# Kernel optimization log

Hardware: AMD Instinct MI355X
Metric: run time of the kernel (lower is better)

## Reference

```python
import jax, jax.numpy as jnp
import numpy as np

B, C, H, W = 8, 512, 96, 96
CQ = 64  # inter_ch


def setup_inputs() -> dict:
    key = jax.random.key(0)
    ks = jax.random.split(key, 8)
    scale = 1.0 / np.sqrt(C)
    return {
        "x": jax.random.normal(ks[0], (B, C, H, W), dtype=jnp.float32),
        "Wq": jax.random.normal(ks[1], (CQ, C), dtype=jnp.float32) * scale,
        "bq": jax.random.normal(ks[2], (CQ,), dtype=jnp.float32) * 0.01,
        "Wk": jax.random.normal(ks[3], (CQ, C), dtype=jnp.float32) * scale,
        "bk": jax.random.normal(ks[4], (CQ,), dtype=jnp.float32) * 0.01,
        "Wv": jax.random.normal(ks[5], (C, C), dtype=jnp.float32) * scale,
        "bv": jax.random.normal(ks[6], (C,), dtype=jnp.float32) * 0.01,
        "gamma": jax.random.normal(ks[7], (1,), dtype=jnp.float32) * 0.1,
    }


def reference(x, Wq, bq, Wk, bk, Wv, bv, gamma):
    # 1x1 convs expressed as channel matmuls; outputs in BHWC layout
    Q = jnp.einsum('bchw,oc->bhwo', x, Wq) + bq   # [B,H,W,CQ]
    K = jnp.einsum('bchw,oc->bhwo', x, Wk) + bk   # [B,H,W,CQ]
    V = jnp.einsum('bchw,oc->bhwo', x, Wv) + bv   # [B,H,W,C]

    # Per pixel (i,j): keys = concat(row i keys [W], column j keys [H]).
    # NOTE: this replication includes pixel (i,j) twice (once in row, once in col),
    # matching the torch loop exactly (no -INF masking as in original CCNet).
    e_row = jnp.einsum('bhwc,bhvc->bhwv', Q, K)   # [B,H,W,W] attend along row h
    e_col = jnp.einsum('bhwc,bgwc->bhwg', Q, K)   # [B,H,W,H] attend along col w
    attn = jax.nn.softmax(jnp.concatenate([e_row, e_col], axis=-1), axis=-1)
    a_row, a_col = attn[..., :W], attn[..., W:]   # [B,H,W,W], [B,H,W,H]

    out = (jnp.einsum('bhwv,bhvc->bhwc', a_row, V)
           + jnp.einsum('bhwg,bgwc->bhwc', a_col, V))  # [B,H,W,C]
    out = jnp.transpose(out, (0, 3, 1, 2))        # [B,C,H,W]
    return x + gamma[0] * out
```

## Files before the change

kernel.cpp:

```cpp
#include <hip/hip_runtime.h>
#include <stdint.h>

#define B_  8
#define C_  512
#define H_  96
#define W_  96
#define CQ_ 64
#define P_  (H_*W_)
#define NP  (B_*P_)
#define L_  (W_+H_)

typedef __attribute__((ext_vector_type(8))) short short8;
typedef __attribute__((ext_vector_type(4))) float f32x4;

__device__ __forceinline__ ushort f2bf(float f) {
    uint32_t u = __builtin_bit_cast(uint32_t, f);
    u += 0x7fff + ((u >> 16) & 1);
    return (ushort)(u >> 16);
}
__device__ __forceinline__ float bf2f(ushort h) {
    uint32_t u = ((uint32_t)h) << 16;
    return __builtin_bit_cast(float, u);
}

__global__ __launch_bounds__(256) void k_xt(const float* __restrict__ x, ushort* __restrict__ xt) {
    __shared__ float tile[64][65];
    int p0 = blockIdx.x * 64, c0 = blockIdx.y * 64, bat = blockIdx.z;
    int tx = threadIdx.x, ty = threadIdx.y;
    const float* xb = x + ((size_t)bat * C_ + c0) * P_ + p0;
    #pragma unroll
    for (int i = ty; i < 64; i += 4) tile[i][tx] = xb[(size_t)i * P_ + tx];
    __syncthreads();
    ushort* o = xt + ((size_t)bat * P_ + p0) * C_ + c0;
    #pragma unroll
    for (int i = ty; i < 64; i += 4) o[(size_t)i * C_ + tx] = f2bf(tile[tx][i]);
}

__global__ __launch_bounds__(256) void k_wconv(const float* __restrict__ Wq, const float* __restrict__ Wk,
                                               const float* __restrict__ Wv, ushort* __restrict__ Wall) {
    int idx = blockIdx.x * 256 + threadIdx.x;
    if (idx >= 640 * C_) return;
    int o = idx / C_, c = idx % C_;
    float v;
    if (o < 64)       v = Wq[o * C_ + c];
    else if (o < 128) v = Wk[(o - 64) * C_ + c];
    else              v = Wv[(o - 128) * C_ + c];
    Wall[idx] = f2bf(v);
}

#define LSTR 40
__global__ __launch_bounds__(256) void k_qk(const ushort* __restrict__ xt, const ushort* __restrict__ Wall,
                                            const float* __restrict__ bq, const float* __restrict__ bk,
                                            ushort* __restrict__ Qb, ushort* __restrict__ Kb) {
    __shared__ __align__(16) ushort Al[128 * LSTR];
    __shared__ __align__(16) ushort Bl[128 * LSTR];
    int tid = threadIdx.x, lane = tid & 63, wvid = tid >> 6;
    int wr = wvid >> 1, wc = wvid & 1;
    int r0 = blockIdx.x * 128;
    f32x4 acc[4][4] = {};
    for (int kb = 0; kb < C_; kb += 32) {
        #pragma unroll
        for (int s = 0; s < 2; ++s) {
            int idx = tid + s * 256, row = idx >> 2, seg = idx & 3;
            *(short8*)&Al[row * LSTR + seg * 8] = *(const short8*)&xt[(size_t)(r0 + row) * C_ + kb + seg * 8];
            *(short8*)&Bl[row * LSTR + seg * 8] = *(const short8*)&Wall[(size_t)row * C_ + kb + seg * 8];
        }
        __syncthreads();
        int rr = lane & 15, gq = lane >> 4;
        #pragma unroll
        for (int mt = 0; mt < 4; ++mt) {
            short8 fa = *(const short8*)&Al[(wr * 64 + mt * 16 + rr) * LSTR + gq * 8];
            #pragma unroll
            for (int nt = 0; nt < 4; ++nt) {
                short8 fb = *(const short8*)&Bl[(wc * 64 + nt * 16 + rr) * LSTR + gq * 8];
                acc[mt][nt] = __builtin_amdgcn_mfma_f32_16x16x32_bf16(fa, fb, acc[mt][nt], 0, 0, 0);
            }
        }
        __syncthreads();
    }
    int rr = lane & 15, gq = lane >> 4;
    #pragma unroll
    for (int mt = 0; mt < 4; ++mt)
        #pragma unroll
        for (int nt = 0; nt < 4; ++nt) {
            int o = wc * 64 + nt * 16 + rr;
            #pragma unroll
            for (int q = 0; q < 4; ++q) {
                size_t prow = (size_t)r0 + wr * 64 + mt * 16 + gq * 4 + q;
                float v = acc[mt][nt][q];
                if (o < 64) Qb[prow * CQ_ + o]        = f2bf(v + bq[o]);
                else        Kb[prow * CQ_ + (o - 64)] = f2bf(v + bk[o - 64]);
            }
        }
}

__global__ __launch_bounds__(256) void k_v(const ushort* __restrict__ xt, const ushort* __restrict__ Wall,
                                           const float* __restrict__ bv, ushort* __restrict__ Vcm) {
    __shared__ __align__(16) ushort Al[128 * LSTR];
    __shared__ __align__(16) ushort Bl[128 * LSTR];
    int tid = threadIdx.x, lane = tid & 63, wvid = tid >> 6;
    int wr = wvid >> 1, wc = wvid & 1;
    int n0 = blockIdx.x * 128;
    int m0 = blockIdx.y * 128;
    f32x4 acc[4][4] = {};
    for (int kb = 0; kb < C_; kb += 32) {
        #pragma unroll
        for (int s = 0; s < 2; ++s) {
            int idx = tid + s * 256, row = idx >> 2, seg = idx & 3;
            *(short8*)&Al[row * LSTR + seg * 8] = *(const short8*)&Wall[(size_t)(128 + m0 + row) * C_ + kb + seg * 8];
            *(short8*)&Bl[row * LSTR + seg * 8] = *(const short8*)&xt[(size_t)(n0 + row) * C_ + kb + seg * 8];
        }
        __syncthreads();
        int rr = lane & 15, gq = lane >> 4;
        #pragma unroll
        for (int mt = 0; mt < 4; ++mt) {
            short8 fa = *(const short8*)&Al[(wr * 64 + mt * 16 + rr) * LSTR + gq * 8];
            #pragma unroll
            for (int nt = 0; nt < 4; ++nt) {
                short8 fb = *(const short8*)&Bl[(wc * 64 + nt * 16 + rr) * LSTR + gq * 8];
                acc[mt][nt] = __builtin_amdgcn_mfma_f32_16x16x32_bf16(fa, fb, acc[mt][nt], 0, 0, 0);
            }
        }
        __syncthreads();
    }
    int rr = lane & 15, gq = lane >> 4;
    int bat = n0 / P_, pb = n0 % P_;
    #pragma unroll
    for (int mt = 0; mt < 4; ++mt)
        #pragma unroll
        for (int nt = 0; nt < 4; ++nt) {
            int pl = pb + wc * 64 + nt * 16 + rr;
            #pragma unroll
            for (int q = 0; q < 4; ++q) {
                int c = m0 + wr * 64 + mt * 16 + gq * 4 + q;
                Vcm[((size_t)(bat * C_ + c)) * P_ + pl] = f2bf(acc[mt][nt][q] + bv[c]);
            }
        }
}

__global__ __launch_bounds__(256) void k_vt(const ushort* __restrict__ Vcm, ushort* __restrict__ Vt) {
    __shared__ ushort t[32][33];
    int tile = blockIdx.x; int h0 = (tile / 3) * 32, w0 = (tile % 3) * 32;
    int c = blockIdx.y, bat = blockIdx.z;
    int tx = threadIdx.x, ty = threadIdx.y;
    const ushort* src = Vcm + ((size_t)(bat * C_ + c)) * P_;
    #pragma unroll
    for (int i = ty; i < 32; i += 8) t[i][tx] = src[(h0 + i) * W_ + w0 + tx];
    __syncthreads();
    #pragma unroll
    for (int i = ty; i < 32; i += 8)
        Vt[((size_t)(bat * W_ + w0 + i) * C_ + c) * H_ + h0 + tx] = t[tx][i];
}

__global__ __launch_bounds__(256) void k_erow(const ushort* __restrict__ Qb, const ushort* __restrict__ Kb,
                                              float* __restrict__ logits) {
    __shared__ __align__(16) ushort Al[96 * LSTR];
    __shared__ __align__(16) ushort Bl[96 * LSTR];
    int h = blockIdx.x, bat = blockIdx.y;
    int tid = threadIdx.x, lane = tid & 63, wvid = tid >> 6;
    int wr = wvid >> 1, wc = wvid & 1;
    size_t base = ((size_t)bat * H_ + h) * W_;
    f32x4 acc[3][3] = {};
    for (int kb = 0; kb < CQ_; kb += 32) {
        for (int s = tid; s < 96 * 4; s += 256) {
            int row = s >> 2, seg = s & 3;
            *(short8*)&Al[row * LSTR + seg * 8] = *(const short8*)&Qb[(base + row) * CQ_ + kb + seg * 8];
            *(short8*)&Bl[row * LSTR + seg * 8] = *(const short8*)&Kb[(base + row) * CQ_ + kb + seg * 8];
        }
        __syncthreads();
        int rr = lane & 15, gq = lane >> 4;
        #pragma unroll
        for (int mt = 0; mt < 3; ++mt) {
            short8 fa = *(const short8*)&Al[(wr * 48 + mt * 16 + rr) * LSTR + gq * 8];
            #pragma unroll
            for (int nt = 0; nt < 3; ++nt) {
                short8 fb = *(const short8*)&Bl[(wc * 48 + nt * 16 + rr) * LSTR + gq * 8];
                acc[mt][nt] = __builtin_amdgcn_mfma_f32_16x16x32_bf16(fa, fb, acc[mt][nt], 0, 0, 0);
            }
        }
        __syncthreads();
    }
    int rr = lane & 15, gq = lane >> 4;
    #pragma unroll
    for (int mt = 0; mt < 3; ++mt)
        #pragma unroll
        for (int nt = 0; nt < 3; ++nt)
            #pragma unroll
            for (int q = 0; q < 4; ++q) {
                int w = wr * 48 + mt * 16 + gq * 4 + q;
                int v = wc * 48 + nt * 16 + rr;
                logits[(base + w) * L_ + v] = acc[mt][nt][q];
            }
}

__global__ __launch_bounds__(256) void k_ecol(const ushort* __restrict__ Qb, const ushort* __restrict__ Kb,
                                              float* __restrict__ logits) {
    __shared__ __align__(16) ushort Al[96 * LSTR];
    __shared__ __align__(16) ushort Bl[96 * LSTR];
    int w = blockIdx.x, bat = blockIdx.y;
    int tid = threadIdx.x, lane = tid & 63, wvid = tid >> 6;
    int wr = wvid >> 1, wc = wvid & 1;
    f32x4 acc[3][3] = {};
    for (int kb = 0; kb < CQ_; kb += 32) {
        for (int s = tid; s < 96 * 4; s += 256) {
            int row = s >> 2, seg = s & 3;
            size_t px = ((size_t)bat * H_ + row) * W_ + w;
            *(short8*)&Al[row * LSTR + seg * 8] = *(const short8*)&Qb[px * CQ_ + kb + seg * 8];
            *(short8*)&Bl[row * LSTR + seg * 8] = *(const short8*)&Kb[px * CQ_ + kb + seg * 8];
        }
        __syncthreads();
        int rr = lane & 15, gq = lane >> 4;
        #pragma unroll
        for (int mt = 0; mt < 3; ++mt) {
            short8 fa = *(const short8*)&Al[(wr * 48 + mt * 16 + rr) * LSTR + gq * 8];
            #pragma unroll
            for (int nt = 0; nt < 3; ++nt) {
                short8 fb = *(const short8*)&Bl[(wc * 48 + nt * 16 + rr) * LSTR + gq * 8];
                acc[mt][nt] = __builtin_amdgcn_mfma_f32_16x16x32_bf16(fa, fb, acc[mt][nt], 0, 0, 0);
            }
        }
        __syncthreads();
    }
    int rr = lane & 15, gq = lane >> 4;
    #pragma unroll
    for (int mt = 0; mt < 3; ++mt)
        #pragma unroll
        for (int nt = 0; nt < 3; ++nt)
            #pragma unroll
            for (int q = 0; q < 4; ++q) {
                int hh = wr * 48 + mt * 16 + gq * 4 + q;
                int gg = wc * 48 + nt * 16 + rr;
                logits[(((size_t)bat * H_ + hh) * W_ + w) * L_ + W_ + gg] = acc[mt][nt][q];
            }
}

__global__ __launch_bounds__(256) void k_softmax(const float* __restrict__ logits, ushort* __restrict__ attn) {
    int wvid = threadIdx.x >> 6, lane = threadIdx.x & 63;
    size_t px = (size_t)blockIdx.x * 4 + wvid;
    const float* lp = logits + px * L_;
    float v0 = lp[lane], v1 = lp[lane + 64], v2 = lp[lane + 128];
    float m = fmaxf(fmaxf(v0, v1), v2);
    #pragma unroll
    for (int off = 32; off; off >>= 1) m = fmaxf(m, __shfl_xor(m, off));
    float e0 = __expf(v0 - m), e1 = __expf(v1 - m), e2 = __expf(v2 - m);
    float s = e0 + e1 + e2;
    #pragma unroll
    for (int off = 32; off; off >>= 1) s += __shfl_xor(s, off);
    float inv = 1.0f / s;
    ushort* ap = attn + px * L_;
    ap[lane] = f2bf(e0 * inv); ap[lane + 64] = f2bf(e1 * inv); ap[lane + 128] = f2bf(e2 * inv);
}

__global__ __launch_bounds__(256) void k_pvrow(const ushort* __restrict__ Vcm, const ushort* __restrict__ attn,
                                               ushort* __restrict__ out0) {
    __shared__ __align__(16) ushort Al[128 * LSTR];
    __shared__ __align__(16) ushort Bl[96 * LSTR];
    int h = blockIdx.x, ct = blockIdx.y, bat = blockIdx.z;
    int tid = threadIdx.x, lane = tid & 63, wvid = tid >> 6;
    int wr = wvid >> 1, wc = wvid & 1;
    int c0 = ct * 128;
    size_t vbase = ((size_t)bat * C_ + c0) * P_ + (size_t)h * W_;
    size_t abase = (((size_t)bat * H_ + h) * W_) * L_;
    f32x4 acc[4][3] = {};
    for (int kb = 0; kb < 96; kb += 32) {
        for (int s = tid; s < 512; s += 256) {
            int row = s >> 2, seg = s & 3;
            *(short8*)&Al[row * LSTR + seg * 8] = *(const short8*)&Vcm[vbase + (size_t)row * P_ + kb + seg * 8];
        }
        for (int s = tid; s < 384; s += 256) {
            int row = s >> 2, seg = s & 3;
            *(short8*)&Bl[row * LSTR + seg * 8] = *(const short8*)&attn[abase + (size_t)row * L_ + kb + seg * 8];
        }
        __syncthreads();
        int rr = lane & 15, gq = lane >> 4;
        #pragma unroll
        for (int mt = 0; mt < 4; ++mt) {
            short8 fa = *(const short8*)&Al[(wr * 64 + mt * 16 + rr) * LSTR + gq * 8];
            #pragma unroll
            for (int nt = 0; nt < 3; ++nt) {
                short8 fb = *(const short8*)&Bl[(wc * 48 + nt * 16 + rr) * LSTR + gq * 8];
                acc[mt][nt] = __builtin_amdgcn_mfma_f32_16x16x32_bf16(fa, fb, acc[mt][nt], 0, 0, 0);
            }
        }
        __syncthreads();
    }
    int rr = lane & 15, gq = lane >> 4;
    #pragma unroll
    for (int mt = 0; mt < 4; ++mt)
        #pragma unroll
        for (int nt = 0; nt < 3; ++nt)
            #pragma unroll
            for (int q = 0; q < 4; ++q) {
                int c = c0 + wr * 64 + mt * 16 + gq * 4 + q;
                int w = wc * 48 + nt * 16 + rr;
                out0[((size_t)bat * C_ + c) * P_ + (size_t)h * W_ + w] = f2bf(acc[mt][nt][q]);
            }
}

__global__ __launch_bounds__(256) void k_pvcol(const ushort* __restrict__ Vt, const ushort* __restrict__ attn,
                                               ushort* __restrict__ out1) {
    __shared__ __align__(16) ushort Al[96 * LSTR];
    __shared__ __align__(16) ushort Bl[128 * LSTR];
    int w = blockIdx.x, ct = blockIdx.y, bat = blockIdx.z;
    int tid = threadIdx.x, lane = tid & 63, wvid = tid >> 6;
    int wr = wvid >> 1, wc = wvid & 1;
    int c0 = ct * 128;
    size_t abase = (((size_t)bat * H_) * W_ + w) * L_ + W_;
    size_t vbase = (((size_t)bat * W_ + w) * C_ + c0) * (size_t)H_;
    f32x4 acc[3][4] = {};
    for (int kb = 0; kb < 96; kb += 32) {
        for (int s = tid; s < 384; s += 256) {
            int row = s >> 2, seg = s & 3;
            *(short8*)&Al[row * LSTR + seg * 8] = *(const short8*)&attn[abase + (size_t)row * (W_ * L_) + kb + seg * 8];
        }
        for (int s = tid; s < 512; s += 256) {
            int row = s >> 2, seg = s & 3;
            *(short8*)&Bl[row * LSTR + seg * 8] = *(const short8*)&Vt[vbase + (size_t)row * H_ + kb + seg * 8];
        }
        __syncthreads();
        int rr = lane & 15, gq = lane >> 4;
        #pragma unroll
        for (int mt = 0; mt < 3; ++mt) {
            short8 fa = *(const short8*)&Al[(wr * 48 + mt * 16 + rr) * LSTR + gq * 8];
            #pragma unroll
            for (int nt = 0; nt < 4; ++nt) {
                short8 fb = *(const short8*)&Bl[(wc * 64 + nt * 16 + rr) * LSTR + gq * 8];
                acc[mt][nt] = __builtin_amdgcn_mfma_f32_16x16x32_bf16(fa, fb, acc[mt][nt], 0, 0, 0);
            }
        }
        __syncthreads();
    }
    int rr = lane & 15, gq = lane >> 4;
    #pragma unroll
    for (int mt = 0; mt < 3; ++mt)
        #pragma unroll
        for (int nt = 0; nt < 4; ++nt)
            #pragma unroll
            for (int q = 0; q < 4; ++q) {
                int hh = wr * 48 + mt * 16 + gq * 4 + q;
                int cc = c0 + wc * 64 + nt * 16 + rr;
                out1[(((size_t)bat * H_ + hh) * W_ + w) * C_ + cc] = f2bf(acc[mt][nt][q]);
            }
}

__global__ __launch_bounds__(256) void k_final(const float* __restrict__ x, const ushort* __restrict__ out0,
                                               const ushort* __restrict__ out1, const float* __restrict__ gamma,
                                               float* __restrict__ out) {
    __shared__ float t[32][33];
    int p0 = blockIdx.x * 32, c0 = blockIdx.y * 32, bat = blockIdx.z;
    int tx = threadIdx.x, ty = threadIdx.y;
    #pragma unroll
    for (int i = ty; i < 32; i += 8)
        t[i][tx] = bf2f(out1[((size_t)bat * P_ + p0 + i) * C_ + c0 + tx]);
    __syncthreads();
    float gm = gamma[0];
    #pragma unroll
    for (int i = ty; i < 32; i += 8) {
        size_t idx = ((size_t)bat * C_ + c0 + i) * P_ + p0 + tx;
        out[idx] = x[idx] + gm * (bf2f(out0[idx]) + t[tx][i]);
    }
}

extern "C" void kernel_launch(void* const* d_in, const int* in_sizes, int n_in,
                              void* d_out, int out_size, void* d_ws, size_t ws_size,
                              hipStream_t stream) {
    const float* x     = (const float*)d_in[0];
    const float* Wq    = (const float*)d_in[1];
    const float* bq    = (const float*)d_in[2];
    const float* Wk    = (const float*)d_in[3];
    const float* bk    = (const float*)d_in[4];
    const float* Wv    = (const float*)d_in[5];
    const float* bv    = (const float*)d_in[6];
    const float* gamma = (const float*)d_in[7];
    float* out = (float*)d_out;
    char* ws = (char*)d_ws;

    const size_t SZ = (size_t)NP * C_ * 2;
    ushort* Qb     = (ushort*)(ws);
    ushort* Kb     = (ushort*)(ws + (size_t)NP * CQ_ * 2);
    float*  logits = (float*) (ws + (size_t)NP * CQ_ * 4);
    ushort* out1   = (ushort*)(ws);
    ushort* xt     = (ushort*)(ws + SZ);
    ushort* out0   = xt;
    ushort* Vcm    = (ushort*)(ws + 2 * SZ);
    ushort* Vt     = (ushort*)(ws + 3 * SZ);
    ushort* attn   = (ushort*)(ws + 4 * SZ);
    ushort* Wall   = (ushort*)(ws + 4 * SZ + (size_t)NP * L_ * 2);

    k_xt     <<<dim3(144, 8, 8),  dim3(64, 4), 0, stream>>>(x, xt);
    k_wconv  <<<dim3(1280),       dim3(256),   0, stream>>>(Wq, Wk, Wv, Wall);
    k_qk     <<<dim3(576),        dim3(256),   0, stream>>>(xt, Wall, bq, bk, Qb, Kb);
    k_v      <<<dim3(576, 4),     dim3(256),   0, stream>>>(xt, Wall, bv, Vcm);
    k_vt     <<<dim3(9, 512, 8),  dim3(32, 8), 0, stream>>>(Vcm, Vt);
    k_erow   <<<dim3(96, 8),      dim3(256),   0, stream>>>(Qb, Kb, logits);
    k_ecol   <<<dim3(96, 8),      dim3(256),   0, stream>>>(Qb, Kb, logits);
    k_softmax<<<dim3(NP / 4),     dim3(256),   0, stream>>>(logits, attn);
    k_pvrow  <<<dim3(96, 4, 8),   dim3(256),   0, stream>>>(Vcm, attn, out0);
    k_pvcol  <<<dim3(96, 4, 8),   dim3(256),   0, stream>>>(Vt, attn, out1);
    k_final  <<<dim3(288, 16, 8), dim3(32, 8), 0, stream>>>(x, out0, out1, gamma, out);
}
```

Baseline: 429.2 us.

## Fuse Q/K/V projections into one GEMM and widen PV tiles to full channels

Merges the separate QK and V projection GEMMs into a single 512-thread kernel that computes all 640 output channels per pixel tile, so xt is read once, and adds a small transpose kernel to restore pixel-major Q/K. The PV row/col kernels now cover all 512 channels per block, which reuses the attention tile across channels. The column output is written channel-major so the final epilogue reads it with a per-channel LDS transpose and vectorized float2 accesses. The xt transpose is also vectorized. The trade-offs are a large accumulator array (10x4 per wave) that raises register pressure, and an extra launch plus the Q/K round trip through memory.

```diff
diff --git a/kernel.cpp b/kernel.cpp
--- a/kernel.cpp
+++ b/kernel.cpp
@@ -29,16 +29,31 @@
     int tx = threadIdx.x, ty = threadIdx.y;
     const float* xb = x + ((size_t)bat * C_ + c0) * P_ + p0;
     #pragma unroll
-    for (int i = ty; i < 64; i += 4) tile[i][tx] = xb[(size_t)i * P_ + tx];
+    for (int i = ty; i < 64; i += 8) {
+        float2 v = *(const float2*)&xb[(size_t)i * P_ + 2 * tx];
+        tile[i][2 * tx] = v.x; tile[i][2 * tx + 1] = v.y;
+    }
     __syncthreads();
     ushort* o = xt + ((size_t)bat * P_ + p0) * C_ + c0;
     #pragma unroll
-    for (int i = ty; i < 64; i += 4) o[(size_t)i * C_ + tx] = f2bf(tile[tx][i]);
+    for (int i = ty; i < 64; i += 8) {
+        ushort2 v; v.x = f2bf(tile[2 * tx][i]); v.y = f2bf(tile[2 * tx + 1][i]);
+        *(ushort2*)&o[(size_t)i * C_ + 2 * tx] = v;
+    }
 }
 
 __global__ __launch_bounds__(256) void k_wconv(const float* __restrict__ Wq, const float* __restrict__ Wk,
-                                               const float* __restrict__ Wv, ushort* __restrict__ Wall) {
+                                               const float* __restrict__ Wv, const float* __restrict__ bq,
+                                               const float* __restrict__ bk, const float* __restrict__ bv,
+                                               ushort* __restrict__ Wall, float* __restrict__ ball) {
     int idx = blockIdx.x * 256 + threadIdx.x;
+    if (idx < 640) {
+        float b;
+        if (idx < 64)       b = bq[idx];
+        else if (idx < 128) b = bk[idx - 64];
+        else                b = bv[idx - 128];
+        ball[idx] = b;
+    }
     if (idx >= 640 * C_) return;
     int o = idx / C_, c = idx % C_;
     float v;
@@ -49,93 +64,70 @@
 }
 
 #define LSTR 40
-__global__ __launch_bounds__(256) void k_qk(const ushort* __restrict__ xt, const ushort* __restrict__ Wall,
-                                            const float* __restrict__ bq, const float* __restrict__ bk,
-                                            ushort* __restrict__ Qb, ushort* __restrict__ Kb) {
-    __shared__ __align__(16) ushort Al[128 * LSTR];
+__global__ __launch_bounds__(512) void k_qkv(const ushort* __restrict__ xt, const ushort* __restrict__ Wall,
+                                             const float* __restrict__ ball,
+                                             ushort* __restrict__ Qcm, ushort* __restrict__ Kcm,
+                                             ushort* __restrict__ Vcm) {
+    __shared__ __align__(16) ushort Al[640 * LSTR];
     __shared__ __align__(16) ushort Bl[128 * LSTR];
     int tid = threadIdx.x, lane = tid & 63, wvid = tid >> 6;
-    int wr = wvid >> 1, wc = wvid & 1;
+    int wrm = wvid >> 1, wcn = wvid & 1;
     int r0 = blockIdx.x * 128;
-    f32x4 acc[4][4] = {};
+    f32x4 acc[10][4] = {};
     for (int kb = 0; kb < C_; kb += 32) {
         #pragma unroll
-        for (int s = 0; s < 2; ++s) {
-            int idx = tid + s * 256, row = idx >> 2, seg = idx & 3;
-            *(short8*)&Al[row * LSTR + seg * 8] = *(const short8*)&xt[(size_t)(r0 + row) * C_ + kb + seg * 8];
-            *(short8*)&Bl[row * LSTR + seg * 8] = *(const short8*)&Wall[(size_t)row * C_ + kb + seg * 8];
+        for (int s = 0; s < 5; ++s) {
+            int idx = tid + s * 512, row = idx >> 2, seg = idx & 3;
+            *(short8*)&Al[row * LSTR + seg * 8] = *(const short8*)&Wall[(size_t)row * C_ + kb + seg * 8];
+        }
+        {
+            int row = tid >> 2, seg = tid & 3;
+            *(short8*)&Bl[row * LSTR + seg * 8] = *(const short8*)&xt[(size_t)(r0 + row) * C_ + kb + seg * 8];
         }
         __syncthreads();
         int rr = lane & 15, gq = lane >> 4;
-        #pragma unroll
-        for (int mt = 0; mt < 4; ++mt) {
-            short8 fa = *(const short8*)&Al[(wr * 64 + mt * 16 + rr) * LSTR + gq * 8];
-            #pragma unroll
-            for (int nt = 0; nt < 4; ++nt) {
-                short8 fb = *(const short8*)&Bl[(wc * 64 + nt * 16 + rr) * LSTR + gq * 8];
-                acc[mt][nt] = __builtin_amdgcn_mfma_f32_16x16x32_bf16(fa, fb, acc[mt][nt], 0, 0, 0);
-            }
+        short8 fb[4];
+        #pragma unroll
+        for (int nt = 0; nt < 4; ++nt) fb[nt] = *(const short8*)&Bl[(wcn * 64 + nt * 16 + rr) * LSTR + gq * 8];
+        #pragma unroll
+        for (int mt = 0; mt < 10; ++mt) {
+            short8 fa = *(const short8*)&Al[(wrm * 160 + mt * 16 + rr) * LSTR + gq * 8];
+            #pragma unroll
+            for (int nt = 0; nt < 4; ++nt)
+                acc[mt][nt] = __builtin_amdgcn_mfma_f32_16x16x32_bf16(fa, fb[nt], acc[mt][nt], 0, 0, 0);
         }
         __syncthreads();
     }
     int rr = lane & 15, gq = lane >> 4;
-    #pragma unroll
-    for (int mt = 0; mt < 4; ++mt)
+    int bat = r0 / P_, pb = r0 % P_;
+    #pragma unroll
+    for (int mt = 0; mt < 10; ++mt)
         #pragma unroll
         for (int nt = 0; nt < 4; ++nt) {
-            int o = wc * 64 + nt * 16 + rr;
+            int col = wcn * 64 + nt * 16 + rr;
             #pragma unroll
             for (int q = 0; q < 4; ++q) {
-                size_t prow = (size_t)r0 + wr * 64 + mt * 16 + gq * 4 + q;
-                float v = acc[mt][nt][q];
-                if (o < 64) Qb[prow * CQ_ + o]        = f2bf(v + bq[o]);
-                else        Kb[prow * CQ_ + (o - 64)] = f2bf(v + bk[o - 64]);
-            }
-        }
-}
-
-__global__ __launch_bounds__(256) void k_v(const ushort* __restrict__ xt, const ushort* __restrict__ Wall,
-                                           const float* __restrict__ bv, ushort* __restrict__ Vcm) {
-    __shared__ __align__(16) ushort Al[128 * LSTR];
-    __shared__ __align__(16) ushort Bl[128 * LSTR];
-    int tid = threadIdx.x, lane = tid & 63, wvid = tid >> 6;
-    int wr = wvid >> 1, wc = wvid & 1;
-    int n0 = blockIdx.x * 128;
-    int m0 = blockIdx.y * 128;
-    f32x4 acc[4][4] = {};
-    for (int kb = 0; kb < C_; kb += 32) {
-        #pragma unroll
-        for (int s = 0; s < 2; ++s) {
-            int idx = tid + s * 256, row = idx >> 2, seg = idx & 3;
-            *(short8*)&Al[row * LSTR + seg * 8] = *(const short8*)&Wall[(size_t)(128 + m0 + row) * C_ + kb + seg * 8];
-            *(short8*)&Bl[row * LSTR + seg * 8] = *(const short8*)&xt[(size_t)(n0 + row) * C_ + kb + seg * 8];
-        }
-        __syncthreads();
-        int rr = lane & 15, gq = lane >> 4;
-        #pragma unroll
-        for (int mt = 0; mt < 4; ++mt) {
-            short8 fa = *(const short8*)&Al[(wr * 64 + mt * 16 + rr) * LSTR + gq * 8];
-            #pragma unroll
-            for (int nt = 0; nt < 4; ++nt) {
-                short8 fb = *(const short8*)&Bl[(wc * 64 + nt * 16 + rr) * LSTR + gq * 8];
-                acc[mt][nt] = __builtin_amdgcn_mfma_f32_16x16x32_bf16(fa, fb, acc[mt][nt], 0, 0, 0);
-            }
-        }
-        __syncthreads();
-    }
-    int rr = lane & 15, gq = lane >> 4;
-    int bat = n0 / P_, pb = n0 % P_;
-    #pragma unroll
-    for (int mt = 0; mt < 4; ++mt)
-        #pragma unroll
-        for (int nt = 0; nt < 4; ++nt) {
-            int pl = pb + wc * 64 + nt * 16 + rr;
-            #pragma unroll
-            for (int q = 0; q < 4; ++q) {
-                int c = m0 + wr * 64 + mt * 16 + gq * 4 + q;
-                Vcm[((size_t)(bat * C_ + c)) * P_ + pl] = f2bf(acc[mt][nt][q] + bv[c]);
-            }
-        }
+                int o = wrm * 160 + mt * 16 + gq * 4 + q;
+                float v = acc[mt][nt][q] + ball[o];
+                if (o < 64)       Qcm[(size_t)o * NP + r0 + col] = f2bf(v);
+                else if (o < 128) Kcm[(size_t)(o - 64) * NP + r0 + col] = f2bf(v);
+                else              Vcm[((size_t)bat * C_ + (o - 128)) * P_ + pb + col] = f2bf(v);
+            }
+        }
+}
+
+__global__ __launch_bounds__(256) void k_qkt(const ushort* __restrict__ Qcm, const ushort* __restrict__ Kcm,
+                                             ushort* __restrict__ Qb, ushort* __restrict__ Kb) {
+    __shared__ ushort t[64][65];
+    int p0 = blockIdx.x * 64;
+    const ushort* src = blockIdx.y ? Kcm : Qcm;
+    ushort* dst = blockIdx.y ? Kb : Qb;
+    int tx = threadIdx.x, ty = threadIdx.y;
+    #pragma unroll
+    for (int i = ty; i < 64; i += 4) t[i][tx] = src[(size_t)i * NP + p0 + tx];
+    __syncthreads();
+    #pragma unroll
+    for (int i = ty; i < 64; i += 4) dst[(size_t)(p0 + i) * CQ_ + tx] = t[tx][i];
 }
 
 __global__ __launch_bounds__(256) void k_vt(const ushort* __restrict__ Vcm, ushort* __restrict__ Vt) {
@@ -251,113 +243,126 @@
     ap[lane] = f2bf(e0 * inv); ap[lane + 64] = f2bf(e1 * inv); ap[lane + 128] = f2bf(e2 * inv);
 }
 
-__global__ __launch_bounds__(256) void k_pvrow(const ushort* __restrict__ Vcm, const ushort* __restrict__ attn,
+__global__ __launch_bounds__(512) void k_pvrow(const ushort* __restrict__ Vcm, const ushort* __restrict__ attn,
                                                ushort* __restrict__ out0) {
-    __shared__ __align__(16) ushort Al[128 * LSTR];
+    __shared__ __align__(16) ushort Al[512 * LSTR];
     __shared__ __align__(16) ushort Bl[96 * LSTR];
-    int h = blockIdx.x, ct = blockIdx.y, bat = blockIdx.z;
+    int h = blockIdx.x, bat = blockIdx.y;
     int tid = threadIdx.x, lane = tid & 63, wvid = tid >> 6;
-    int wr = wvid >> 1, wc = wvid & 1;
-    int c0 = ct * 128;
-    size_t vbase = ((size_t)bat * C_ + c0) * P_ + (size_t)h * W_;
-    size_t abase = (((size_t)bat * H_ + h) * W_) * L_;
-    f32x4 acc[4][3] = {};
+    int wrm = wvid >> 1, wcn = wvid & 1;
+    size_t vbase = (size_t)bat * C_ * P_ + (size_t)h * W_;
+    size_t abase = ((size_t)bat * H_ + h) * W_ * L_;
+    f32x4 acc[8][3] = {};
     for (int kb = 0; kb < 96; kb += 32) {
-        for (int s = tid; s < 512; s += 256) {
-            int row = s >> 2, seg = s & 3;
+        #pragma unroll
+        for (int s = 0; s < 4; ++s) {
+            int idx = tid + s * 512, row = idx >> 2, seg = idx & 3;
             *(short8*)&Al[row * LSTR + seg * 8] = *(const short8*)&Vcm[vbase + (size_t)row * P_ + kb + seg * 8];
         }
-        for (int s = tid; s < 384; s += 256) {
-            int row = s >> 2, seg = s & 3;
+        if (tid < 384) {
+            int row = tid >> 2, seg = tid & 3;
             *(short8*)&Bl[row * LSTR + seg * 8] = *(const short8*)&attn[abase + (size_t)row * L_ + kb + seg * 8];
         }
         __syncthreads();
         int rr = lane & 15, gq = lane >> 4;
-        #pragma unroll
-        for (int mt = 0; mt < 4; ++mt) {
-            short8 fa = *(const short8*)&Al[(wr * 64 + mt * 16 + rr) * LSTR + gq * 8];
-            #pragma unroll
-            for (int nt = 0; nt < 3; ++nt) {
-                short8 fb = *(const short8*)&Bl[(wc * 48 + nt * 16 + rr) * LSTR + gq * 8];
-                acc[mt][nt] = __builtin_amdgcn_mfma_f32_16x16x32_bf16(fa, fb, acc[mt][nt], 0, 0, 0);
-            }
+        short8 fb[3];
+        #pragma unroll
+        for (int nt = 0; nt < 3; ++nt) fb[nt] = *(const short8*)&Bl[(wcn * 48 + nt * 16 + rr) * LSTR + gq * 8];
+        #pragma unroll
+        for (int mt = 0; mt < 8; ++mt) {
+            short8 fa = *(const short8*)&Al[(wrm * 128 + mt * 16 + rr) * LSTR + gq * 8];
+            #pragma unroll
+            for (int nt = 0; nt < 3; ++nt)
+                acc[mt][nt] = __builtin_amdgcn_mfma_f32_16x16x32_bf16(fa, fb[nt], acc[mt][nt], 0, 0, 0);
         }
         __syncthreads();
     }
     int rr = lane & 15, gq = lane >> 4;
     #pragma unroll
-    for (int mt = 0; mt < 4; ++mt)
-        #pragma unroll
-        for (int nt = 0; nt < 3; ++nt)
+    for (int mt = 0; mt < 8; ++mt)
+        #pragma unroll
+        for (int nt = 0; nt < 3; ++nt) {
+            int w = wcn * 48 + nt * 16 + rr;
             #pragma unroll
             for (int q = 0; q < 4; ++q) {
-                int c = c0 + wr * 64 + mt * 16 + gq * 4 + q;
-                int w = wc * 48 + nt * 16 + rr;
+                int c = wrm * 128 + mt * 16 + gq * 4 + q;
                 out0[((size_t)bat * C_ + c) * P_ + (size_t)h * W_ + w] = f2bf(acc[mt][nt][q]);
             }
-}
-
-__global__ __launch_bounds__(256) void k_pvcol(const ushort* __restrict__ Vt, const ushort* __restrict__ attn,
-                                               ushort* __restrict__ out1) {
-    __shared__ __align__(16) ushort Al[96 * LSTR];
-    __shared__ __align__(16) ushort Bl[128 * LSTR];
-    int w = blockIdx.x, ct = blockIdx.y, bat = blockIdx.z;
+        }
+}
+
+__global__ __launch_bounds__(512) void k_pvcol(const ushort* __restrict__ Vt, const ushort* __restrict__ attn,
+                                               ushort* __restrict__ out1t) {
+    __shared__ __align__(16) ushort Al[512 * LSTR];
+    __shared__ __align__(16) ushort Bl[96 * LSTR];
+    int w = blockIdx.x, bat = blockIdx.y;
     int tid = threadIdx.x, lane = tid & 63, wvid = tid >> 6;
-    int wr = wvid >> 1, wc = wvid & 1;
-    int c0 = ct * 128;
-    size_t abase = (((size_t)bat * H_) * W_ + w) * L_ + W_;
-    size_t vbase = (((size_t)bat * W_ + w) * C_ + c0) * (size_t)H_;
-    f32x4 acc[3][4] = {};
+    int wrm = wvid >> 1, wcn = wvid & 1;
+    size_t vbase = ((size_t)bat * W_ + w) * C_ * H_;
+    size_t abase = ((size_t)bat * P_ + w) * L_ + W_;
+    f32x4 acc[8][3] = {};
     for (int kb = 0; kb < 96; kb += 32) {
-        for (int s = tid; s < 384; s += 256) {
-            int row = s >> 2, seg = s & 3;
-            *(short8*)&Al[row * LSTR + seg * 8] = *(const short8*)&attn[abase + (size_t)row * (W_ * L_) + kb + seg * 8];
-        }
-        for (int s = tid; s < 512; s += 256) {
-            int row = s >> 2, seg = s & 3;
-            *(short8*)&Bl[row * LSTR + seg * 8] = *(const short8*)&Vt[vbase + (size_t)row * H_ + kb + seg * 8];
+        #pragma unroll
+        for (int s = 0; s < 4; ++s) {
+            int idx = tid + s * 512, row = idx >> 2, seg = idx & 3;
+            *(short8*)&Al[row * LSTR + seg * 8] = *(const short8*)&Vt[vbase + (size_t)row * H_ + kb + seg * 8];
+        }
+        if (tid < 384) {
+            int row = tid >> 2, seg = tid & 3;
+            *(short8*)&Bl[row * LSTR + seg * 8] = *(const short8*)&attn[abase + (size_t)row * (W_ * L_) + kb + seg * 8];
         }
         __syncthreads();
         int rr = lane & 15, gq = lane >> 4;
-        #pragma unroll
-        for (int mt = 0; mt < 3; ++mt) {
-            short8 fa = *(const short8*)&Al[(wr * 48 + mt * 16 + rr) * LSTR + gq * 8];
-            #pragma unroll
-            for (int nt = 0; nt < 4; ++nt) {
-                short8 fb = *(const short8*)&Bl[(wc * 64 + nt * 16 + rr) * LSTR + gq * 8];
-                acc[mt][nt] = __builtin_amdgcn_mfma_f32_16x16x32_bf16(fa, fb, acc[mt][nt], 0, 0, 0);
-            }
+        short8 fb[3];
+        #pragma unroll
+        for (int nt = 0; nt < 3; ++nt) fb[nt] = *(const short8*)&Bl[(wcn * 48 + nt * 16 + rr) * LSTR + gq * 8];
+        #pragma unroll
+        for (int mt = 0; mt < 8; ++mt) {
+            short8 fa = *(const short8*)&Al[(wrm * 128 + mt * 16 + rr) * LSTR + gq * 8];
+            #pragma unroll
+            for (int nt = 0; nt < 3; ++nt)
+                acc[mt][nt] = __builtin_amdgcn_mfma_f32_16x16x32_bf16(fa, fb[nt], acc[mt][nt], 0, 0, 0);
         }
         __syncthreads();
     }
     int rr = lane & 15, gq = lane >> 4;
     #pragma unroll
-    for (int mt = 0; mt < 3; ++mt)
-        #pragma unroll
-        for (int nt = 0; nt < 4; ++nt)
+    for (int mt = 0; mt < 8; ++mt)
+        #pragma unroll
+        for (int nt = 0; nt < 3; ++nt) {
+            int hh = wcn * 48 + nt * 16 + rr;
             #pragma unroll
             for (int q = 0; q < 4; ++q) {
-                int hh = wr * 48 + mt * 16 + gq * 4 + q;
-                int cc = c0 + wc * 64 + nt * 16 + rr;
-                out1[(((size_t)bat * H_ + hh) * W_ + w) * C_ + cc] = f2bf(acc[mt][nt][q]);
-            }
+                int c = wrm * 128 + mt * 16 + gq * 4 + q;
+                out1t[((size_t)(bat * C_ + c) * W_ + w) * H_ + hh] = f2bf(acc[mt][nt][q]);
+            }
+        }
 }
 
 __global__ __launch_bounds__(256) void k_final(const float* __restrict__ x, const ushort* __restrict__ out0,
-                                               const ushort* __restrict__ out1, const float* __restrict__ gamma,
+                                               const ushort* __restrict__ out1t, const float* __restrict__ gamma,
                                                float* __restrict__ out) {
-    __shared__ float t[32][33];
-    int p0 = blockIdx.x * 32, c0 = blockIdx.y * 32, bat = blockIdx.z;
-    int tx = threadIdx.x, ty = threadIdx.y;
-    #pragma unroll
-    for (int i = ty; i < 32; i += 8)
-        t[i][tx] = bf2f(out1[((size_t)bat * P_ + p0 + i) * C_ + c0 + tx]);
+    __shared__ ushort t[96 * 98];
+    int c = blockIdx.x, bat = blockIdx.y;
+    const ushort* src = out1t + ((size_t)bat * C_ + c) * P_;
+    int tid = threadIdx.x;
+    for (int i = tid; i < 4608; i += 256) {
+        int w = i / 48, h = (i % 48) * 2;
+        ushort2 v = *(const ushort2*)&src[w * 96 + h];
+        *(ushort2*)&t[w * 98 + h] = v;
+    }
     __syncthreads();
     float gm = gamma[0];
-    #pragma unroll
-    for (int i = ty; i < 32; i += 8) {
-        size_t idx = ((size_t)bat * C_ + c0 + i) * P_ + p0 + tx;
-        out[idx] = x[idx] + gm * (bf2f(out0[idx]) + t[tx][i]);
+    size_t base = ((size_t)bat * C_ + c) * P_;
+    for (int i = tid; i < 4608; i += 256) {
+        int h = i / 48, w = (i % 48) * 2;
+        size_t idx = base + h * W_ + w;
+        float2 xv = *(const float2*)&x[idx];
+        ushort2 o0 = *(const ushort2*)&out0[idx];
+        float2 r;
+        r.x = xv.x + gm * (bf2f(o0.x) + bf2f(t[w * 98 + h]));
+        r.y = xv.y + gm * (bf2f(o0.y) + bf2f(t[(w + 1) * 98 + h]));
+        *(float2*)&out[idx] = r;
     }
 }
 
@@ -375,27 +380,31 @@
     float* out = (float*)d_out;
     char* ws = (char*)d_ws;
 
-    const size_t SZ = (size_t)NP * C_ * 2;
-    ushort* Qb     = (ushort*)(ws);
-    ushort* Kb     = (ushort*)(ws + (size_t)NP * CQ_ * 2);
-    float*  logits = (float*) (ws + (size_t)NP * CQ_ * 4);
-    ushort* out1   = (ushort*)(ws);
+    const size_t SZ  = (size_t)NP * C_ * 2;
+    const size_t QKS = (size_t)NP * CQ_ * 2;
+    ushort* Qcm    = (ushort*)(ws);
+    ushort* Kcm    = (ushort*)(ws + QKS);
+    float*  logits = (float*) (ws + 2 * QKS);
+    ushort* out1t  = (ushort*)(ws);
     ushort* xt     = (ushort*)(ws + SZ);
     ushort* out0   = xt;
     ushort* Vcm    = (ushort*)(ws + 2 * SZ);
     ushort* Vt     = (ushort*)(ws + 3 * SZ);
+    ushort* Qb     = (ushort*)(ws + 4 * SZ);
+    ushort* Kb     = (ushort*)(ws + 4 * SZ + QKS);
     ushort* attn   = (ushort*)(ws + 4 * SZ);
     ushort* Wall   = (ushort*)(ws + 4 * SZ + (size_t)NP * L_ * 2);
-
-    k_xt     <<<dim3(144, 8, 8),  dim3(64, 4), 0, stream>>>(x, xt);
-    k_wconv  <<<dim3(1280),       dim3(256),   0, stream>>>(Wq, Wk, Wv, Wall);
-    k_qk     <<<dim3(576),        dim3(256),   0, stream>>>(xt, Wall, bq, bk, Qb, Kb);
-    k_v      <<<dim3(576, 4),     dim3(256),   0, stream>>>(xt, Wall, bv, Vcm);
+    float*  ball   = (float*) (ws + 4 * SZ + (size_t)NP * L_ * 2 + 640 * C_ * 2);
+
+    k_xt     <<<dim3(144, 8, 8),  dim3(32, 8), 0, stream>>>(x, xt);
+    k_wconv  <<<dim3(1280),       dim3(256),   0, stream>>>(Wq, Wk, Wv, bq, bk, bv, Wall, ball);
+    k_qkv    <<<dim3(576),        dim3(512),   0, stream>>>(xt, Wall, ball, Qcm, Kcm, Vcm);
+    k_qkt    <<<dim3(1152, 2),    dim3(64, 4), 0, stream>>>(Qcm, Kcm, Qb, Kb);
     k_vt     <<<dim3(9, 512, 8),  dim3(32, 8), 0, stream>>>(Vcm, Vt);
     k_erow   <<<dim3(96, 8),      dim3(256),   0, stream>>>(Qb, Kb, logits);
     k_ecol   <<<dim3(96, 8),      dim3(256),   0, stream>>>(Qb, Kb, logits);
     k_softmax<<<dim3(NP / 4),     dim3(256),   0, stream>>>(logits, attn);
-    k_pvrow  <<<dim3(96, 4, 8),   dim3(256),   0, stream>>>(Vcm, attn, out0);
-    k_pvcol  <<<dim3(96, 4, 8),   dim3(256),   0, stream>>>(Vt, attn, out1);
-    k_final  <<<dim3(288, 16, 8), dim3(32, 8), 0, stream>>>(x, out0, out1, gamma, out);
-}
+    k_pvrow  <<<dim3(96, 8),      dim3(512),   0, stream>>>(Vcm, attn, out0);
+    k_pvcol  <<<dim3(96, 8),      dim3(512),   0, stream>>>(Vt, attn, out1t);
+    k_final  <<<dim3(512, 8),     dim3(256),   0, stream>>>(x, out0, out1t, gamma, out);
+}
```

After: 428.7 us. Within noise of the previous version (-0.1%).
